# Kernel tuning notes

Measured on AMD Instinct MI355X. Metric: run time of the kernel, lower is better.

The kernel has to match this reference:

```python
import jax, jax.numpy as jnp
import numpy as np

B, L = 32, 512
D_EMB = 500      # tagger_mlp_layer
LANG = 100       # tagger_embeddings_size
H = 800          # tagger_encoder_size * 2
P_ARC = 100      # parser_arc_proj_size
P_LAB = 400      # parser_label_proj_size
MLP = 500        # tagger_mlp_layer (aux_mlp out)
N_LANG, N_LAB, N_UPOS, N_XPOS, N_ATTRS = 8, 50, 20, 300, 500


def setup_inputs() -> dict:
    key = jax.random.key(0)
    ks = jax.random.split(key, 24)
    s = 0.05
    lang_table = jax.random.normal(ks[3], (N_LANG, LANG), jnp.float32) * s
    lang_table = lang_table.at[0].set(0.0)  # padding_idx=0
    return {
        "emb": jax.random.normal(ks[0], (B, L, D_EMB), jnp.float32),
        "hidden": jax.random.normal(ks[1], (B, L, H), jnp.float32),
        "lang_ids": jax.random.randint(ks[2], (B,), 0, N_LANG),
        "lang_table": lang_table,
        "W_arc": jax.random.normal(ks[4], (P_ARC, D_EMB + LANG), jnp.float32) * s,
        "b_arc": jax.random.normal(ks[5], (P_ARC,), jnp.float32) * s,
        "W_lab": jax.random.normal(ks[6], (P_LAB, D_EMB + LANG), jnp.float32) * s,
        "b_lab": jax.random.normal(ks[7], (P_LAB,), jnp.float32) * s,
        "w_head": jax.random.normal(ks[8], (2 * P_ARC,), jnp.float32) * s,
        "b_head": jax.random.normal(ks[9], (1,), jnp.float32) * s,
        "W_aux": jax.random.normal(ks[10], (MLP, H), jnp.float32) * s,
        "b_aux": jax.random.normal(ks[11], (MLP,), jnp.float32) * s,
        "W_upos": jax.random.normal(ks[12], (N_UPOS, MLP + LANG), jnp.float32) * s,
        "b_upos": jax.random.normal(ks[13], (N_UPOS,), jnp.float32) * s,
        "W_xpos": jax.random.normal(ks[14], (N_XPOS, MLP + LANG), jnp.float32) * s,
        "b_xpos": jax.random.normal(ks[15], (N_XPOS,), jnp.float32) * s,
        "W_attrs": jax.random.normal(ks[16], (N_ATTRS, MLP + LANG), jnp.float32) * s,
        "b_attrs": jax.random.normal(ks[17], (N_ATTRS,), jnp.float32) * s,
    }


def reference(emb, hidden, lang_ids, lang_table, W_arc, b_arc, W_lab, b_lab,
              w_head, b_head, W_aux, b_aux, W_upos, b_upos, W_xpos, b_xpos,
              W_attrs, b_attrs):
    Bv, Lv = emb.shape[0], emb.shape[1]
    lang_emb = lang_table[lang_ids]                              # [B, LANG]
    lang_rep = jnp.broadcast_to(lang_emb[:, None, :], (Bv, Lv, lang_emb.shape[-1]))
    ho = jnp.concatenate((emb, lang_rep), axis=2)                # [B, L, D_EMB+LANG]

    proj_arc = jnp.tanh(jnp.einsum('bld,pd->blp', ho, W_arc) + b_arc)   # [B, L, P_ARC]
    proj_label = jnp.tanh(jnp.einsum('bld,pd->blp', ho, W_lab) + b_lab) # [B, L, P_LAB]

    # Biaffine decomposition of output_head(cat(pa[i], pa[j])):
    # score(i,j) = pa[i] . w1 + pa[j] . w2 + b
    P = proj_arc.shape[-1]
    s1 = proj_arc @ w_head[:P]                                   # [B, L]
    s2 = proj_arc @ w_head[P:]                                   # [B, L]
    core = s1[:, :, None] + s2[:, None, :] + b_head[0]           # [B, L, L]
    arcs = jnp.concatenate(
        (jnp.zeros((Bv, Lv, 1), core.dtype), core), axis=2)     # [B, L, L+1]

    aux_hid = jnp.tanh(jnp.einsum('blh,mh->blm', hidden, W_aux) + b_aux)  # [B, L, MLP]
    aux_cat = jnp.concatenate((aux_hid, lang_rep), axis=2)
    s_upos = jnp.einsum('blm,um->blu', aux_cat, W_upos) + b_upos
    s_xpos = jnp.einsum('blm,um->blu', aux_cat, W_xpos) + b_xpos
    s_attrs = jnp.einsum('blm,um->blu', aux_cat, W_attrs) + b_attrs
    return arcs, proj_label, s_upos, s_xpos, s_attrs
```

## Files before the change

### kernel.cpp

```cpp
#include <hip/hip_runtime.h>


using f16   = _Float16;
using f16x4 = __attribute__((ext_vector_type(4))) _Float16;
using f16x8 = __attribute__((ext_vector_type(8))) _Float16;
using f32x4 = __attribute__((ext_vector_type(4))) float;

#define M_ROWS 16384

__device__ __forceinline__ f16 f2h(float f) { return (f16)f; }
__device__ __forceinline__ f16x4 cvt4(float4 v) {
  return f16x4{ f2h(v.x), f2h(v.y), f2h(v.z), f2h(v.w) };
}

__device__ __forceinline__ float fast_tanh(float x) {
  float xc = fminf(fmaxf(x, -15.f), 15.f);
  float e  = __builtin_amdgcn_exp2f(xc * 2.885390081777927f);
  return 1.f - 2.f * __builtin_amdgcn_rcpf(e + 1.f);
}

__device__ __forceinline__ void async16(void* lds, const void* gp) {
  __builtin_amdgcn_global_load_lds(
      (const __attribute__((address_space(1))) unsigned int*)gp,
      (__attribute__((address_space(3))) unsigned int*)lds, 16, 0, 0);
}

__global__ __launch_bounds__(256) void setup_kernel(
    const float* __restrict__ emb, const float* __restrict__ hidden,
    const float* __restrict__ lang_table, const int* __restrict__ lang_ids,
    const float* __restrict__ W_arc, const float* __restrict__ b_arc,
    const float* __restrict__ W_lab, const float* __restrict__ b_lab,
    const float* __restrict__ W_aux, const float* __restrict__ b_aux,
    const float* __restrict__ W_upos, const float* __restrict__ b_upos,
    const float* __restrict__ W_xpos, const float* __restrict__ b_xpos,
    const float* __restrict__ W_attrs, const float* __restrict__ b_attrs,
    f16* __restrict__ ho, f16* __restrict__ aux_cat, f16* __restrict__ hid16,
    f16* __restrict__ W_proj, f16* __restrict__ W_auxp, f16* __restrict__ W_heads,
    float* __restrict__ bias_proj, float* __restrict__ bias_aux, float* __restrict__ bias_heads)
{
  const int HID_Q = 3276800;
  const int HO_Q  = 2621440;
  const int W_Q   = 327680;
  const int TOTAL = HID_Q + HO_Q + W_Q;

  for (int q = blockIdx.x * 256 + threadIdx.x; q < TOTAL; q += gridDim.x * 256) {
    if (q < HID_Q) {
      float4 v = *(const float4*)(hidden + 4 * (size_t)q);
      *(f16x4*)(hid16 + 4 * (size_t)q) = cvt4(v);
    } else if (q < HID_Q + HO_Q) {
      int p = q - HID_Q;
      int row = p / 160;
      int s = p - row * 160;
      f16* horow = ho + (size_t)row * 640;
      if (s < 125) {
        float4 v = *(const float4*)(emb + (size_t)row * 500 + 4 * s);
        *(f16x4*)(horow + 4 * s) = cvt4(v);
      } else {
        f16x4 h = { (f16)0.f, (f16)0.f, (f16)0.f, (f16)0.f };
        if (s < 150) {
          const float* lrow = lang_table + (size_t)lang_ids[row >> 9] * 100;
          float4 v = *(const float4*)(lrow + (s - 125) * 4);
          h = cvt4(v);
        }
        *(f16x4*)(horow + 4 * s) = h;
        *(f16x4*)(aux_cat + (size_t)row * 640 + 4 * s) = h;
      }
    } else {
      int w = q - (HID_Q + HO_Q);
      const float* src = nullptr;
      f16* dst;
      if (w < 81920) {
        int n = w / 160, s = w - n * 160;
        dst = W_proj + (size_t)w * 4;
        if (s < 150 && n < 500)
          src = (n < 100 ? W_arc + (size_t)n * 600
                         : W_lab + (size_t)(n - 100) * 600) + s * 4;
      } else if (w < 184320) {
        int w2 = w - 81920;
        int n = w2 / 200;
        dst = W_auxp + (size_t)w2 * 4;
        if (n < 500) src = W_aux + (size_t)w2 * 4;
      } else {
        int w3 = w - 184320;
        int n = w3 / 160, s = w3 - n * 160;
        dst = W_heads + (size_t)w3 * 4;
        if (s < 150 && n < 820)
          src = (n < 20 ? W_upos + (size_t)n * 600
                : n < 320 ? W_xpos + (size_t)(n - 20) * 600
                          : W_attrs + (size_t)(n - 320) * 600) + s * 4;
      }
      f16x4 h = { (f16)0.f, (f16)0.f, (f16)0.f, (f16)0.f };
      if (src) h = cvt4(*(const float4*)src);
      *(f16x4*)dst = h;
    }
  }

  if (blockIdx.x == 0) {
    for (int idx = threadIdx.x; idx < 1920; idx += 256) {
      if (idx < 512) {
        float v = 0.f;
        if (idx < 100)      v = b_arc[idx];
        else if (idx < 500) v = b_lab[idx - 100];
        bias_proj[idx] = v;
      } else if (idx < 1024) {
        int i = idx - 512;
        bias_aux[i] = (i < 500) ? b_aux[i] : 0.f;
      } else {
        int i = idx - 1024; float v = 0.f;
        if (i < 20)       v = b_upos[i];
        else if (i < 320) v = b_xpos[i - 20];
        else if (i < 820) v = b_attrs[i - 320];
        bias_heads[i] = v;
      }
    }
  }
}

__device__ __forceinline__ void gemm_core(
    const f16* __restrict__ A, const f16* __restrict__ B, const int K,
    const int bm, const int bn,
    f16 (*ldsA)[128 * 32], f16 (*ldsB)[128 * 32], f32x4 (&acc)[4][4])
{
  const int tid  = threadIdx.x;
  const int lane = tid & 63;
  const int wave = tid >> 6;
  const int wm = wave >> 1, wn = wave & 1;
  const int m16 = lane & 15, quad = lane >> 4;

  const int q0 = tid, q1 = tid + 256;
  const f16* gA0 = A + (size_t)(bm * 128 + (q0 >> 2)) * K + (q0 & 3) * 8;
  const f16* gA1 = A + (size_t)(bm * 128 + (q1 >> 2)) * K + (q1 & 3) * 8;
  const f16* gB0 = B + (size_t)(bn * 128 + (q0 >> 2)) * K + (q0 & 3) * 8;
  const f16* gB1 = B + (size_t)(bn * 128 + (q1 >> 2)) * K + (q1 & 3) * 8;

#define STAGE(buf, k0) do {                                        \
    async16(&((uint4*)ldsA[buf])[wave * 64],       gA0 + (k0));    \
    async16(&((uint4*)ldsA[buf])[wave * 64 + 256], gA1 + (k0));    \
    async16(&((uint4*)ldsB[buf])[wave * 64],       gB0 + (k0));    \
    async16(&((uint4*)ldsB[buf])[wave * 64 + 256], gB1 + (k0));    \
  } while (0)

#define COMPUTE(buf) do {                                                        \
    f16x8 af[4], bfr[4];                                                         \
    _Pragma("unroll")                                                            \
    for (int i = 0; i < 4; ++i)                                                  \
      af[i] = *(const f16x8*)&ldsA[buf][(wm * 64 + i * 16 + m16) * 32 + quad * 8]; \
    _Pragma("unroll")                                                            \
    for (int j = 0; j < 4; ++j)                                                  \
      bfr[j] = *(const f16x8*)&ldsB[buf][(wn * 64 + j * 16 + m16) * 32 + quad * 8]; \
    _Pragma("unroll")                                                            \
    for (int i = 0; i < 4; ++i)                                                  \
      _Pragma("unroll")                                                          \
      for (int j = 0; j < 4; ++j)                                                \
        acc[i][j] = __builtin_amdgcn_mfma_f32_16x16x32_f16(af[i], bfr[j], acc[i][j], 0, 0, 0); \
  } while (0)

  const int NT = K >> 5;
  STAGE(0, 0);
  STAGE(1, 32);
  asm volatile("s_waitcnt vmcnt(4)" ::: "memory");
  __builtin_amdgcn_s_barrier();
  __builtin_amdgcn_sched_barrier(0);

  int c0 = 0, c1 = 1, c2 = 2;
  for (int t = 0; t < NT; ++t) {
    if (t + 2 < NT) STAGE(c2, (t + 2) << 5);
    COMPUTE(c0);
    if (t + 1 < NT) {
      if (t + 2 < NT) asm volatile("s_waitcnt vmcnt(4)" ::: "memory");
      else            asm volatile("s_waitcnt vmcnt(0)" ::: "memory");
      __builtin_amdgcn_s_barrier();
      __builtin_amdgcn_sched_barrier(0);
      int tmp = c0; c0 = c1; c1 = c2; c2 = tmp;
    }
  }
#undef STAGE
#undef COMPUTE
}

__global__ __launch_bounds__(256) void gemm01(
    const f16* __restrict__ ho, const f16* __restrict__ hid16,
    const f16* __restrict__ W_proj, const f16* __restrict__ W_auxp,
    const float* __restrict__ bias_proj, const float* __restrict__ bias_aux,
    float* __restrict__ out_label, const float* __restrict__ w_head,
    float* __restrict__ s1, float* __restrict__ s2, f16* __restrict__ aux_cat)
{
  __shared__ __align__(16) f16 ldsA[3][128 * 32];
  __shared__ __align__(16) f16 ldsB[3][128 * 32];
  __shared__ float s1red[2][128], s2red[2][128];

  const int tid  = threadIdx.x;
  const int lane = tid & 63;
  const int wave = tid >> 6;
  const int wm = wave >> 1, wn = wave & 1;
  const int m16 = lane & 15, quad = lane >> 4;
  const int bm  = blockIdx.x;
  const int bny = blockIdx.y;
  const bool is0 = (bny < 4);
  const int bn  = is0 ? bny : bny - 4;

  const f16* A = is0 ? ho : hid16;
  const f16* B = is0 ? W_proj : W_auxp;
  const float* bias = is0 ? bias_proj : bias_aux;
  const int K = is0 ? 640 : 800;

  f32x4 acc[4][4] = {};
  gemm_core(A, B, K, bm, bn, ldsA, ldsB, acc);

  const int row0 = bm * 128 + wm * 64 + quad * 4;
  const int col0 = bn * 128 + wn * 64 + m16;

  if (is0) {
    float p1[4][4] = {}, p2[4][4] = {};
    const bool isbn0 = (bn == 0);
#pragma unroll
    for (int i = 0; i < 4; ++i) {
#pragma unroll
      for (int j = 0; j < 4; ++j) {
        const int col = col0 + j * 16;
        const float bcol = bias[col];
        float w1c = 0.f, w2c = 0.f;
        if (isbn0 && col < 100) { w1c = w_head[col]; w2c = w_head[100 + col]; }
#pragma unroll
        for (int r = 0; r < 4; ++r) {
          const int row = row0 + i * 16 + r;
          float v = fast_tanh(acc[i][j][r] + bcol);
          if (col >= 100 && col < 500) out_label[(size_t)row * 400 + col - 100] = v;
          p1[i][r] += v * w1c;
          p2[i][r] += v * w2c;
        }
      }
    }
    if (isbn0) {
#pragma unroll
      for (int d = 1; d < 16; d <<= 1) {
#pragma unroll
        for (int i = 0; i < 4; ++i)
#pragma unroll
          for (int r = 0; r < 4; ++r) {
            p1[i][r] += __shfl_xor(p1[i][r], d);
            p2[i][r] += __shfl_xor(p2[i][r], d);
          }
      }
      if (m16 == 0) {
#pragma unroll
        for (int i = 0; i < 4; ++i)
#pragma unroll
          for (int r = 0; r < 4; ++r) {
            int rl = wm * 64 + i * 16 + quad * 4 + r;
            s1red[wn][rl] = p1[i][r];
            s2red[wn][rl] = p2[i][r];
          }
      }
      __syncthreads();
      if (tid < 128)       s1[bm * 128 + tid] = s1red[0][tid] + s1red[1][tid];
      else                 s2[bm * 128 + tid - 128] = s2red[0][tid - 128] + s2red[1][tid - 128];
    }
  } else {
#pragma unroll
    for (int i = 0; i < 4; ++i)
#pragma unroll
      for (int j = 0; j < 4; ++j) {
        const int col = col0 + j * 16;
        const float bcol = bias[col];
#pragma unroll
        for (int r = 0; r < 4; ++r) {
          const int row = row0 + i * 16 + r;
          if (col < 500) aux_cat[(size_t)row * 640 + col] = f2h(fast_tanh(acc[i][j][r] + bcol));
        }
      }
  }
}

__global__ __launch_bounds__(256) void gemm2_arcs(
    const f16* __restrict__ aux_cat, const f16* __restrict__ W_heads,
    const float* __restrict__ bias_heads,
    const float* __restrict__ s1, const float* __restrict__ s2,
    const float* __restrict__ b_head,
    float* __restrict__ out_arcs, float* __restrict__ out_upos,
    float* __restrict__ out_xpos, float* __restrict__ out_attrs)
{
  __shared__ __align__(16) f16 ldsA[3][128 * 32];
  __shared__ __align__(16) f16 ldsB[3][128 * 32];
  __shared__ float s2s[512];

  const int bm = blockIdx.x, bn = blockIdx.y;

  if (bn == 7) {
    const int r0 = bm * 128;
    const int b = r0 >> 9;
    const float bh = b_head[0];
    for (int j = threadIdx.x; j < 512; j += 256) s2s[j] = s2[(b << 9) + j];
    __syncthreads();
    for (int rr = 0; rr < 128; ++rr) {
      const int row = r0 + rr;
      const float s1v = s1[row] + bh;
      float* orow = out_arcs + (size_t)row * 513;
      if (threadIdx.x == 0) orow[0] = 0.f;
#pragma unroll
      for (int j = threadIdx.x; j < 512; j += 256)
        orow[1 + j] = s1v + s2s[j];
    }
    return;
  }

  const int tid  = threadIdx.x;
  const int lane = tid & 63;
  const int wave = tid >> 6;
  const int wm = wave >> 1, wn = wave & 1;
  const int m16 = lane & 15, quad = lane >> 4;

  f32x4 acc[4][4] = {};
  gemm_core(aux_cat, W_heads, 640, bm, bn, ldsA, ldsB, acc);

  const int row0 = bm * 128 + wm * 64 + quad * 4;
  const int col0 = bn * 128 + wn * 64 + m16;
#pragma unroll
  for (int i = 0; i < 4; ++i)
#pragma unroll
    for (int j = 0; j < 4; ++j) {
      const int col = col0 + j * 16;
      const float bcol = bias_heads[col];
#pragma unroll
      for (int r = 0; r < 4; ++r) {
        const int row = row0 + i * 16 + r;
        float v = acc[i][j][r] + bcol;
        if (col < 20)        out_upos[(size_t)row * 20 + col] = v;
        else if (col < 320)  out_xpos[(size_t)row * 300 + col - 20] = v;
        else if (col < 820)  out_attrs[(size_t)row * 500 + col - 320] = v;
      }
    }
}

extern "C" void kernel_launch(void* const* d_in, const int* in_sizes, int n_in,
                              void* d_out, int out_size, void* d_ws, size_t ws_size,
                              hipStream_t stream)
{
  const float* emb      = (const float*)d_in[0];
  const float* hidden   = (const float*)d_in[1];
  const int*   lang_ids = (const int*)d_in[2];
  const float* lang_tab = (const float*)d_in[3];
  const float* W_arc  = (const float*)d_in[4];
  const float* b_arc  = (const float*)d_in[5];
  const float* W_lab  = (const float*)d_in[6];
  const float* b_lab  = (const float*)d_in[7];
  const float* w_head = (const float*)d_in[8];
  const float* b_head = (const float*)d_in[9];
  const float* W_aux  = (const float*)d_in[10];
  const float* b_aux  = (const float*)d_in[11];
  const float* W_upos = (const float*)d_in[12];
  const float* b_upos = (const float*)d_in[13];
  const float* W_xpos = (const float*)d_in[14];
  const float* b_xpos = (const float*)d_in[15];
  const float* W_attrs = (const float*)d_in[16];
  const float* b_attrs = (const float*)d_in[17];

  char* ws = (char*)d_ws;
  f16* ho      = (f16*)(ws + 0);
  f16* aux_cat = (f16*)(ws + 20971520);
  f16* hid16   = (f16*)(ws + 41943040);
  f16* W_proj  = (f16*)(ws + 68157440);
  f16* W_auxp  = (f16*)(ws + 68812800);
  f16* W_heads = (f16*)(ws + 69632000);
  float* bias_proj  = (float*)(ws + 70778880);
  float* bias_aux   = (float*)(ws + 70780928);
  float* bias_heads = (float*)(ws + 70782976);
  float* s1         = (float*)(ws + 70786560);
  float* s2         = (float*)(ws + 70852096);

  float* out       = (float*)d_out;
  float* out_arcs  = out;
  float* out_label = out + 8404992;
  float* out_upos  = out + 14958592;
  float* out_xpos  = out + 15286272;
  float* out_attrs = out + 20201472;

  setup_kernel<<<2048, 256, 0, stream>>>(
      emb, hidden, lang_tab, lang_ids,
      W_arc, b_arc, W_lab, b_lab, W_aux, b_aux,
      W_upos, b_upos, W_xpos, b_xpos, W_attrs, b_attrs,
      ho, aux_cat, hid16, W_proj, W_auxp, W_heads,
      bias_proj, bias_aux, bias_heads);

  gemm01<<<dim3(128, 8), 256, 0, stream>>>(
      ho, hid16, W_proj, W_auxp, bias_proj, bias_aux,
      out_label, w_head, s1, s2, aux_cat);

  gemm2_arcs<<<dim3(128, 8), 256, 0, stream>>>(
      aux_cat, W_heads, bias_heads, s1, s2, b_head,
      out_arcs, out_upos, out_xpos, out_attrs);
}
```

Before: 322.2 us.

## Enlarge GEMM tiles to 256x256 with 8-wave blocks and swizzled LDS pipeline

Replaces the 128x128, 4-wave, 3-stage GEMM core with a 256x256 tile, 8-wave, double-buffered core. It uses K=64 steps, an XOR-swizzled LDS layout, interleaved async loads and s_setprio around the MFMA groups. The hidden and W_aux matrices are padded to K=832 to fit the 64-wide K steps. The arcs broadcast work is moved from a dedicated block column into every gemm2 block. Larger tiles raise data reuse and cut global/LDS traffic per FLOP, but the grid drops to 256 blocks and register pressure rises, so fewer blocks may fill the 256 CUs and padding waste on the N dimension grows.

```diff
diff --git a/kernel.cpp b/kernel.cpp
--- a/kernel.cpp
+++ b/kernel.cpp
@@ -5,8 +5,6 @@
 using f16x4 = __attribute__((ext_vector_type(4))) _Float16;
 using f16x8 = __attribute__((ext_vector_type(8))) _Float16;
 using f32x4 = __attribute__((ext_vector_type(4))) float;
-
-#define M_ROWS 16384
 
 __device__ __forceinline__ f16 f2h(float f) { return (f16)f; }
 __device__ __forceinline__ f16x4 cvt4(float4 v) {
@@ -38,19 +36,20 @@
     f16* __restrict__ W_proj, f16* __restrict__ W_auxp, f16* __restrict__ W_heads,
     float* __restrict__ bias_proj, float* __restrict__ bias_aux, float* __restrict__ bias_heads)
 {
-  const int HID_Q = 3276800;
-  const int HO_Q  = 2621440;
-  const int W_Q   = 327680;
+  const int HID_Q = 16384 * 208;
+  const int HO_Q  = 16384 * 160;
+  const int W_Q   = 81920 + 106496 + 163840;
   const int TOTAL = HID_Q + HO_Q + W_Q;
 
   for (int q = blockIdx.x * 256 + threadIdx.x; q < TOTAL; q += gridDim.x * 256) {
     if (q < HID_Q) {
-      float4 v = *(const float4*)(hidden + 4 * (size_t)q);
-      *(f16x4*)(hid16 + 4 * (size_t)q) = cvt4(v);
+      int row = q / 208, s = q - row * 208;
+      f16x4 h = { (f16)0.f, (f16)0.f, (f16)0.f, (f16)0.f };
+      if (s < 200) h = cvt4(*(const float4*)(hidden + (size_t)row * 800 + 4 * s));
+      *(f16x4*)(hid16 + (size_t)row * 832 + 4 * s) = h;
     } else if (q < HID_Q + HO_Q) {
       int p = q - HID_Q;
-      int row = p / 160;
-      int s = p - row * 160;
+      int row = p / 160, s = p - row * 160;
       f16* horow = ho + (size_t)row * 640;
       if (s < 125) {
         float4 v = *(const float4*)(emb + (size_t)row * 500 + 4 * s);
@@ -59,8 +58,7 @@
         f16x4 h = { (f16)0.f, (f16)0.f, (f16)0.f, (f16)0.f };
         if (s < 150) {
           const float* lrow = lang_table + (size_t)lang_ids[row >> 9] * 100;
-          float4 v = *(const float4*)(lrow + (s - 125) * 4);
-          h = cvt4(v);
+          h = cvt4(*(const float4*)(lrow + (s - 125) * 4));
         }
         *(f16x4*)(horow + 4 * s) = h;
         *(f16x4*)(aux_cat + (size_t)row * 640 + 4 * s) = h;
@@ -75,13 +73,13 @@
         if (s < 150 && n < 500)
           src = (n < 100 ? W_arc + (size_t)n * 600
                          : W_lab + (size_t)(n - 100) * 600) + s * 4;
-      } else if (w < 184320) {
+      } else if (w < 81920 + 106496) {
         int w2 = w - 81920;
-        int n = w2 / 200;
+        int n = w2 / 208, s = w2 - n * 208;
         dst = W_auxp + (size_t)w2 * 4;
-        if (n < 500) src = W_aux + (size_t)w2 * 4;
+        if (s < 200 && n < 500) src = W_aux + (size_t)n * 800 + s * 4;
       } else {
-        int w3 = w - 184320;
+        int w3 = w - (81920 + 106496);
         int n = w3 / 160, s = w3 - n * 160;
         dst = W_heads + (size_t)w3 * 4;
         if (s < 150 && n < 820)
@@ -96,7 +94,7 @@
   }
 
   if (blockIdx.x == 0) {
-    for (int idx = threadIdx.x; idx < 1920; idx += 256) {
+    for (int idx = threadIdx.x; idx < 2048; idx += 256) {
       if (idx < 512) {
         float v = 0.f;
         if (idx < 100)      v = b_arc[idx];
@@ -116,163 +114,203 @@
   }
 }
 
-__device__ __forceinline__ void gemm_core(
-    const f16* __restrict__ A, const f16* __restrict__ B, const int K,
-    const int bm, const int bn,
-    f16 (*ldsA)[128 * 32], f16 (*ldsB)[128 * 32], f32x4 (&acc)[4][4])
+__device__ __forceinline__ void gemm_core256(
+    const f16* __restrict__ A, const f16* __restrict__ Bm,
+    const int K, const int NT, const int bm, const int bn,
+    f16* __restrict__ ldsA, f16* __restrict__ ldsB, f32x4 (&acc)[8][4])
 {
   const int tid  = threadIdx.x;
   const int lane = tid & 63;
   const int wave = tid >> 6;
-  const int wm = wave >> 1, wn = wave & 1;
+  const int wm = wave >> 2, wn = wave & 3;
   const int m16 = lane & 15, quad = lane >> 4;
 
-  const int q0 = tid, q1 = tid + 256;
-  const f16* gA0 = A + (size_t)(bm * 128 + (q0 >> 2)) * K + (q0 & 3) * 8;
-  const f16* gA1 = A + (size_t)(bm * 128 + (q1 >> 2)) * K + (q1 & 3) * 8;
-  const f16* gB0 = B + (size_t)(bn * 128 + (q0 >> 2)) * K + (q0 & 3) * 8;
-  const f16* gB1 = B + (size_t)(bn * 128 + (q1 >> 2)) * K + (q1 & 3) * 8;
-
-#define STAGE(buf, k0) do {                                        \
-    async16(&((uint4*)ldsA[buf])[wave * 64],       gA0 + (k0));    \
-    async16(&((uint4*)ldsA[buf])[wave * 64 + 256], gA1 + (k0));    \
-    async16(&((uint4*)ldsB[buf])[wave * 64],       gB0 + (k0));    \
-    async16(&((uint4*)ldsB[buf])[wave * 64 + 256], gB1 + (k0));    \
-  } while (0)
-
-#define COMPUTE(buf) do {                                                        \
-    f16x8 af[4], bfr[4];                                                         \
-    _Pragma("unroll")                                                            \
-    for (int i = 0; i < 4; ++i)                                                  \
-      af[i] = *(const f16x8*)&ldsA[buf][(wm * 64 + i * 16 + m16) * 32 + quad * 8]; \
-    _Pragma("unroll")                                                            \
-    for (int j = 0; j < 4; ++j)                                                  \
-      bfr[j] = *(const f16x8*)&ldsB[buf][(wn * 64 + j * 16 + m16) * 32 + quad * 8]; \
-    _Pragma("unroll")                                                            \
-    for (int i = 0; i < 4; ++i)                                                  \
-      _Pragma("unroll")                                                          \
-      for (int j = 0; j < 4; ++j)                                                \
-        acc[i][j] = __builtin_amdgcn_mfma_f32_16x16x32_f16(af[i], bfr[j], acc[i][j], 0, 0, 0); \
-  } while (0)
-
-  const int NT = K >> 5;
-  STAGE(0, 0);
-  STAGE(1, 32);
-  asm volatile("s_waitcnt vmcnt(4)" ::: "memory");
-  __builtin_amdgcn_s_barrier();
-  __builtin_amdgcn_sched_barrier(0);
-
-  int c0 = 0, c1 = 1, c2 = 2;
+  const int sr = lane >> 3;
+  const int ss = (lane & 7) ^ sr;
+  const f16* gA[4]; const f16* gB[4];
+#pragma unroll
+  for (int i = 0; i < 4; ++i) {
+    gA[i] = A  + (size_t)(bm * 256 + i * 64 + wave * 8 + sr) * K + ss * 8;
+    gB[i] = Bm + (size_t)(bn * 256 + i * 64 + wave * 8 + sr) * K + ss * 8;
+  }
+  f16* sA = ldsA + wave * 512;
+  f16* sB = ldsB + wave * 512;
+
+  const int aBase = (wm * 128 + m16) * 64;
+  const int bBase = (wn * 64  + m16) * 64;
+  const int sw0 = ((quad)     ^ (m16 & 7)) * 8;
+  const int sw1 = ((4 | quad) ^ (m16 & 7)) * 8;
+
+  f16x8 af[4], bf[4];
+
+#define RDA(mqv, sw) { _Pragma("unroll")                                        \
+  for (int ii = 0; ii < 4; ++ii)                                                \
+    af[ii] = *(const f16x8*)&ldsA[buf + aBase + (mqv) * 4096 + ii * 1024 + (sw)]; }
+#define RDB(sw) { _Pragma("unroll")                                             \
+  for (int j = 0; j < 4; ++j)                                                   \
+    bf[j] = *(const f16x8*)&ldsB[buf + bBase + j * 1024 + (sw)]; }
+#define MM(mqv) { _Pragma("unroll")                                             \
+  for (int ii = 0; ii < 4; ++ii) { _Pragma("unroll")                            \
+    for (int j = 0; j < 4; ++j)                                                 \
+      acc[(mqv) * 4 + ii][j] = __builtin_amdgcn_mfma_f32_16x16x32_f16(          \
+          af[ii], bf[j], acc[(mqv) * 4 + ii][j], 0, 0, 0); } }
+#define VM2 { asm volatile("s_waitcnt vmcnt(2)" ::: "memory");                  \
+              __builtin_amdgcn_sched_barrier(0); }
+#define VM0 { asm volatile("s_waitcnt vmcnt(0)" ::: "memory");                  \
+              __builtin_amdgcn_sched_barrier(0); }
+#define BAR  __builtin_amdgcn_s_barrier()
+#define PRIO1 __builtin_amdgcn_s_setprio(1)
+#define PRIO0 __builtin_amdgcn_s_setprio(0)
+
+#pragma unroll
+  for (int i = 0; i < 4; ++i) async16(sB + i * 4096, gB[i]);
+#pragma unroll
+  for (int i = 0; i < 4; ++i) async16(sA + i * 4096, gA[i]);
+  VM0;
+  BAR;
+
   for (int t = 0; t < NT; ++t) {
-    if (t + 2 < NT) STAGE(c2, (t + 2) << 5);
-    COMPUTE(c0);
-    if (t + 1 < NT) {
-      if (t + 2 < NT) asm volatile("s_waitcnt vmcnt(4)" ::: "memory");
-      else            asm volatile("s_waitcnt vmcnt(0)" ::: "memory");
-      __builtin_amdgcn_s_barrier();
-      __builtin_amdgcn_sched_barrier(0);
-      int tmp = c0; c0 = c1; c1 = c2; c2 = tmp;
-    }
-  }
-#undef STAGE
-#undef COMPUTE
-}
-
-__global__ __launch_bounds__(256) void gemm01(
+    const int buf = (t & 1) << 14;
+    const int nbf = ((t + 1) & 1) << 14;
+    const bool st = (t + 1 < NT);
+    const int k0n = (t + 1) << 6;
+
+    if (st) { async16(sB + nbf + 0 * 4096, gB[0] + k0n);
+              async16(sB + nbf + 1 * 4096, gB[1] + k0n); }
+    RDB(sw0); RDA(0, sw0);
+    BAR;
+    PRIO1; MM(0); PRIO0;
+    if (t > 0) { if (st) VM2 else VM0 }
+    BAR;
+    if (st) { async16(sB + nbf + 2 * 4096, gB[2] + k0n);
+              async16(sB + nbf + 3 * 4096, gB[3] + k0n); }
+    RDA(1, sw0);
+    BAR;
+    PRIO1; MM(1); PRIO0;
+    BAR;
+    if (st) { async16(sA + nbf + 0 * 4096, gA[0] + k0n);
+              async16(sA + nbf + 2 * 4096, gA[2] + k0n); }
+    RDB(sw1); RDA(0, sw1);
+    BAR;
+    PRIO1; MM(0); PRIO0;
+    BAR;
+    if (st) { async16(sA + nbf + 1 * 4096, gA[1] + k0n);
+              async16(sA + nbf + 3 * 4096, gA[3] + k0n); }
+    RDA(1, sw1);
+    BAR;
+    PRIO1; MM(1); PRIO0;
+    if (st) VM2;
+    BAR;
+  }
+#undef RDA
+#undef RDB
+#undef MM
+#undef VM2
+#undef VM0
+#undef BAR
+#undef PRIO1
+#undef PRIO0
+}
+
+__global__ __launch_bounds__(512, 2) void gemm01(
     const f16* __restrict__ ho, const f16* __restrict__ hid16,
     const f16* __restrict__ W_proj, const f16* __restrict__ W_auxp,
     const float* __restrict__ bias_proj, const float* __restrict__ bias_aux,
     float* __restrict__ out_label, const float* __restrict__ w_head,
     float* __restrict__ s1, float* __restrict__ s2, f16* __restrict__ aux_cat)
 {
-  __shared__ __align__(16) f16 ldsA[3][128 * 32];
-  __shared__ __align__(16) f16 ldsB[3][128 * 32];
-  __shared__ float s1red[2][128], s2red[2][128];
+  __shared__ __align__(16) f16 ldsA[2 * 16384];
+  __shared__ __align__(16) f16 ldsB[2 * 16384];
+  __shared__ float s1red[2][256], s2red[2][256];
 
   const int tid  = threadIdx.x;
   const int lane = tid & 63;
   const int wave = tid >> 6;
-  const int wm = wave >> 1, wn = wave & 1;
+  const int wm = wave >> 2, wn = wave & 3;
   const int m16 = lane & 15, quad = lane >> 4;
   const int bm  = blockIdx.x;
   const int bny = blockIdx.y;
-  const bool is0 = (bny < 4);
-  const int bn  = is0 ? bny : bny - 4;
+  const bool is0 = (bny < 2);
+  const int bn  = is0 ? bny : bny - 2;
 
   const f16* A = is0 ? ho : hid16;
   const f16* B = is0 ? W_proj : W_auxp;
   const float* bias = is0 ? bias_proj : bias_aux;
-  const int K = is0 ? 640 : 800;
-
-  f32x4 acc[4][4] = {};
-  gemm_core(A, B, K, bm, bn, ldsA, ldsB, acc);
-
-  const int row0 = bm * 128 + wm * 64 + quad * 4;
-  const int col0 = bn * 128 + wn * 64 + m16;
+  const int K  = is0 ? 640 : 832;
+  const int NT = is0 ? 10 : 13;
+
+  f32x4 acc[8][4] = {};
+  gemm_core256(A, B, K, NT, bm, bn, ldsA, ldsB, acc);
+
+  const int row0 = bm * 256 + wm * 128 + quad * 4;
+  const int colT = bn * 256 + wn * 64 + m16;
 
   if (is0) {
-    float p1[4][4] = {}, p2[4][4] = {};
-    const bool isbn0 = (bn == 0);
-#pragma unroll
-    for (int i = 0; i < 4; ++i) {
+    float p1[8][4] = {}, p2[8][4] = {};
+    const bool haveHead = (bn == 0);
+#pragma unroll
+    for (int ai = 0; ai < 8; ++ai) {
 #pragma unroll
       for (int j = 0; j < 4; ++j) {
-        const int col = col0 + j * 16;
+        const int col = colT + j * 16;
         const float bcol = bias[col];
         float w1c = 0.f, w2c = 0.f;
-        if (isbn0 && col < 100) { w1c = w_head[col]; w2c = w_head[100 + col]; }
+        if (haveHead && col < 100) { w1c = w_head[col]; w2c = w_head[100 + col]; }
 #pragma unroll
         for (int r = 0; r < 4; ++r) {
-          const int row = row0 + i * 16 + r;
-          float v = fast_tanh(acc[i][j][r] + bcol);
+          const int row = row0 + ai * 16 + r;
+          float v = fast_tanh(acc[ai][j][r] + bcol);
           if (col >= 100 && col < 500) out_label[(size_t)row * 400 + col - 100] = v;
-          p1[i][r] += v * w1c;
-          p2[i][r] += v * w2c;
+          p1[ai][r] += v * w1c;
+          p2[ai][r] += v * w2c;
         }
       }
     }
-    if (isbn0) {
-#pragma unroll
-      for (int d = 1; d < 16; d <<= 1) {
-#pragma unroll
-        for (int i = 0; i < 4; ++i)
-#pragma unroll
-          for (int r = 0; r < 4; ++r) {
-            p1[i][r] += __shfl_xor(p1[i][r], d);
-            p2[i][r] += __shfl_xor(p2[i][r], d);
-          }
-      }
-      if (m16 == 0) {
-#pragma unroll
-        for (int i = 0; i < 4; ++i)
-#pragma unroll
-          for (int r = 0; r < 4; ++r) {
-            int rl = wm * 64 + i * 16 + quad * 4 + r;
-            s1red[wn][rl] = p1[i][r];
-            s2red[wn][rl] = p2[i][r];
-          }
+    if (haveHead) {
+      if (wn < 2) {
+#pragma unroll
+        for (int d = 1; d < 16; d <<= 1)
+#pragma unroll
+          for (int ai = 0; ai < 8; ++ai)
+#pragma unroll
+            for (int r = 0; r < 4; ++r) {
+              p1[ai][r] += __shfl_xor(p1[ai][r], d);
+              p2[ai][r] += __shfl_xor(p2[ai][r], d);
+            }
+        if (m16 == 0) {
+#pragma unroll
+          for (int ai = 0; ai < 8; ++ai)
+#pragma unroll
+            for (int r = 0; r < 4; ++r) {
+              int rl = wm * 128 + ai * 16 + quad * 4 + r;
+              s1red[wn][rl] = p1[ai][r];
+              s2red[wn][rl] = p2[ai][r];
+            }
+        }
       }
       __syncthreads();
-      if (tid < 128)       s1[bm * 128 + tid] = s1red[0][tid] + s1red[1][tid];
-      else                 s2[bm * 128 + tid - 128] = s2red[0][tid - 128] + s2red[1][tid - 128];
+      if (tid < 256) s1[bm * 256 + tid] = s1red[0][tid] + s1red[1][tid];
+      else { int t2 = tid - 256; s2[bm * 256 + t2] = s2red[0][t2] + s2red[1][t2]; }
     }
   } else {
 #pragma unroll
-    for (int i = 0; i < 4; ++i)
+    for (int ai = 0; ai < 8; ++ai)
 #pragma unroll
       for (int j = 0; j < 4; ++j) {
-        const int col = col0 + j * 16;
-        const float bcol = bias[col];
-#pragma unroll
-        for (int r = 0; r < 4; ++r) {
-          const int row = row0 + i * 16 + r;
-          if (col < 500) aux_cat[(size_t)row * 640 + col] = f2h(fast_tanh(acc[i][j][r] + bcol));
+        const int col = colT + j * 16;
+        if (col < 500) {
+          const float bcol = bias[col];
+#pragma unroll
+          for (int r = 0; r < 4; ++r) {
+            const int row = row0 + ai * 16 + r;
+            aux_cat[(size_t)row * 640 + col] = f2h(fast_tanh(acc[ai][j][r] + bcol));
+          }
         }
       }
   }
 }
 
-__global__ __launch_bounds__(256) void gemm2_arcs(
+__global__ __launch_bounds__(512, 2) void gemm2_arcs(
     const f16* __restrict__ aux_cat, const f16* __restrict__ W_heads,
     const float* __restrict__ bias_heads,
     const float* __restrict__ s1, const float* __restrict__ s2,
@@ -280,56 +318,47 @@
     float* __restrict__ out_arcs, float* __restrict__ out_upos,
     float* __restrict__ out_xpos, float* __restrict__ out_attrs)
 {
-  __shared__ __align__(16) f16 ldsA[3][128 * 32];
-  __shared__ __align__(16) f16 ldsB[3][128 * 32];
-  __shared__ float s2s[512];
-
-  const int bm = blockIdx.x, bn = blockIdx.y;
-
-  if (bn == 7) {
-    const int r0 = bm * 128;
-    const int b = r0 >> 9;
-    const float bh = b_head[0];
-    for (int j = threadIdx.x; j < 512; j += 256) s2s[j] = s2[(b << 9) + j];
-    __syncthreads();
-    for (int rr = 0; rr < 128; ++rr) {
-      const int row = r0 + rr;
-      const float s1v = s1[row] + bh;
-      float* orow = out_arcs + (size_t)row * 513;
-      if (threadIdx.x == 0) orow[0] = 0.f;
-#pragma unroll
-      for (int j = threadIdx.x; j < 512; j += 256)
-        orow[1 + j] = s1v + s2s[j];
-    }
-    return;
-  }
+  __shared__ __align__(16) f16 ldsA[2 * 16384];
+  __shared__ __align__(16) f16 ldsB[2 * 16384];
 
   const int tid  = threadIdx.x;
   const int lane = tid & 63;
   const int wave = tid >> 6;
-  const int wm = wave >> 1, wn = wave & 1;
+  const int wm = wave >> 2, wn = wave & 3;
   const int m16 = lane & 15, quad = lane >> 4;
-
-  f32x4 acc[4][4] = {};
-  gemm_core(aux_cat, W_heads, 640, bm, bn, ldsA, ldsB, acc);
-
-  const int row0 = bm * 128 + wm * 64 + quad * 4;
-  const int col0 = bn * 128 + wn * 64 + m16;
-#pragma unroll
-  for (int i = 0; i < 4; ++i)
+  const int bm = blockIdx.x, bn = blockIdx.y;
+
+  f32x4 acc[8][4] = {};
+  gemm_core256(aux_cat, W_heads, 640, 10, bm, bn, ldsA, ldsB, acc);
+
+  const int row0 = bm * 256 + wm * 128 + quad * 4;
+  const int colT = bn * 256 + wn * 64 + m16;
+#pragma unroll
+  for (int ai = 0; ai < 8; ++ai)
 #pragma unroll
     for (int j = 0; j < 4; ++j) {
-      const int col = col0 + j * 16;
+      const int col = colT + j * 16;
       const float bcol = bias_heads[col];
 #pragma unroll
       for (int r = 0; r < 4; ++r) {
-        const int row = row0 + i * 16 + r;
-        float v = acc[i][j][r] + bcol;
+        const int row = row0 + ai * 16 + r;
+        float v = acc[ai][j][r] + bcol;
         if (col < 20)        out_upos[(size_t)row * 20 + col] = v;
         else if (col < 320)  out_xpos[(size_t)row * 300 + col - 20] = v;
         else if (col < 820)  out_attrs[(size_t)row * 500 + col - 320] = v;
       }
     }
+
+  const int r0 = bm * 256 + bn * 64;
+  const float bh = b_head[0];
+  const float s2v = s2[((r0 >> 9) << 9) + tid];
+  for (int rl = 0; rl < 64; ++rl) {
+    const int row = r0 + rl;
+    const float s1v = s1[row] + bh;
+    float* orow = out_arcs + (size_t)row * 513;
+    if (tid == 0) orow[0] = 0.f;
+    orow[1 + tid] = s1v + s2v;
+  }
 }
 
 extern "C" void kernel_launch(void* const* d_in, const int* in_sizes, int n_in,
@@ -359,14 +388,14 @@
   f16* ho      = (f16*)(ws + 0);
   f16* aux_cat = (f16*)(ws + 20971520);
   f16* hid16   = (f16*)(ws + 41943040);
-  f16* W_proj  = (f16*)(ws + 68157440);
-  f16* W_auxp  = (f16*)(ws + 68812800);
-  f16* W_heads = (f16*)(ws + 69632000);
-  float* bias_proj  = (float*)(ws + 70778880);
-  float* bias_aux   = (float*)(ws + 70780928);
-  float* bias_heads = (float*)(ws + 70782976);
-  float* s1         = (float*)(ws + 70786560);
-  float* s2         = (float*)(ws + 70852096);
+  f16* W_proj  = (f16*)(ws + 69206016);
+  f16* W_auxp  = (f16*)(ws + 69861376);
+  f16* W_heads = (f16*)(ws + 70713344);
+  float* bias_proj  = (float*)(ws + 72024064);
+  float* bias_aux   = (float*)(ws + 72026112);
+  float* bias_heads = (float*)(ws + 72028160);
+  float* s1         = (float*)(ws + 72032256);
+  float* s2         = (float*)(ws + 72097792);
 
   float* out       = (float*)d_out;
   float* out_arcs  = out;
@@ -382,11 +411,11 @@
       ho, aux_cat, hid16, W_proj, W_auxp, W_heads,
       bias_proj, bias_aux, bias_heads);
 
-  gemm01<<<dim3(128, 8), 256, 0, stream>>>(
+  gemm01<<<dim3(64, 4), 512, 0, stream>>>(
       ho, hid16, W_proj, W_auxp, bias_proj, bias_aux,
       out_label, w_head, s1, s2, aux_cat);
 
-  gemm2_arcs<<<dim3(128, 8), 256, 0, stream>>>(
+  gemm2_arcs<<<dim3(64, 4), 512, 0, stream>>>(
       aux_cat, W_heads, bias_heads, s1, s2, b_head,
       out_arcs, out_upos, out_xpos, out_attrs);
 }
```

Result: faster. 299.0 us (-7.2%).
